# Optimization experiments

Hardware: AMD Instinct MI355X
Metric: run time of the kernel (lower is better)

Reference implementation:

```python
import jax, jax.numpy as jnp
import numpy as np

# dims: batch, time, in-feat, nodes, hidden, out-feat, filter taps, readout widths
BATCH, T, F, N, H, G = 8, 64, 8, 4096, 32, 32
K1, K2 = 3, 3
R1, R2 = 64, 8


def lsigf(h, S, x):
    """K-tap graph filter (LSIGF, E=1): h (Fout,K,Fin), S (N,N), x (B,Fin,N) -> (B,Fout,N)."""
    K = h.shape[1]
    xs = [x]
    for _ in range(K - 1):  # K is small and static
        xs.append(jnp.einsum('nm,bfm->bfn', S, xs[-1]))
    xk = jnp.stack(xs, axis=1)  # B,K,Fin,N
    return jnp.einsum('gkf,bkfn->bgn', h, xk)


def setup_inputs() -> dict:
    key = jax.random.key(0)
    ks = jax.random.split(key, 20)
    def p(k, shape, scale):
        return jax.random.normal(k, shape, dtype=jnp.float32) * scale
    x = jax.random.normal(ks[0], (BATCH, T, F, N), dtype=jnp.float32)
    z0 = jax.random.normal(ks[1], (BATCH, H, N), dtype=jnp.float32)  # random initial hidden state
    S = jax.random.normal(ks[2], (N, N), dtype=jnp.float32) / jnp.sqrt(jnp.float32(N))  # GSO, O(1) spectral norm
    sA = 1.0 / np.sqrt(K1 * F); sB = 1.0 / np.sqrt(K1 * H); sO = 1.0 / np.sqrt(K2 * H)
    return dict(
        x=x, z0=z0, S=S,
        # main hidden-state filters
        A=p(ks[3], (H, K1, F), sA), Bw=p(ks[4], (H, K1, H), sB), bz=p(ks[5], (H, 1), 0.1),
        # input (update) time-gate filters
        Ca=p(ks[6], (H, K1, F), sA), Cb=p(ks[7], (H, K1, H), sB), bc=p(ks[8], (H, 1), 0.1),
        # forget time-gate filters
        Da=p(ks[9], (H, K1, F), sA), Db=p(ks[10], (H, K1, H), sB), bd=p(ks[11], (H, 1), 0.1),
        # output graph filter
        Wout=p(ks[12], (G, K2, H), sO), bout=p(ks[13], (G, 1), 0.1),
        # local per-node readout MLP G -> R1 -> R2
        W1=p(ks[14], (R1, G), 1.0 / np.sqrt(G)), b1=p(ks[15], (R1,), 0.1),
        W2=p(ks[16], (R2, R1), 1.0 / np.sqrt(R1)), b2=p(ks[17], (R2,), 0.1),
    )


def reference(x, z0, S, A, Bw, bz, Ca, Cb, bc, Da, Db, bd, Wout, bout, W1, b1, W2, b2):
    Bsz = x.shape[0]
    xt_seq = jnp.moveaxis(x, 1, 0)  # T,B,F,N

    def step(z, xt):
        # scalar-per-(batch,time) gates: sigmoid of gate graph filters, pooled over nodes+features
        u = jax.nn.sigmoid(lsigf(Ca, S, xt) + lsigf(Cb, S, z) + bc).mean(axis=(1, 2))[:, None, None]
        f = jax.nn.sigmoid(lsigf(Da, S, xt) + lsigf(Db, S, z) + bd).mean(axis=(1, 2))[:, None, None]
        znew = jnp.tanh(u * lsigf(A, S, xt) + f * lsigf(Bw, S, z) + bz)
        return znew, znew

    _, zs = jax.lax.scan(step, z0, xt_seq)  # T,B,H,N
    z = jnp.moveaxis(zs, 0, 1).reshape(Bsz * T, H, N)
    yOut = jnp.tanh(lsigf(Wout, S, z) + bout).reshape(Bsz, T, G, N)  # nonlinearityOutput = tanh
    y = jnp.moveaxis(yOut, 2, 3)  # B,T,N,G  (local per-node readout)
    y = jax.nn.relu(y @ W1.T + b1) @ W2.T + b2  # B,T,N,R2
    return jnp.moveaxis(y, 3, 2)  # B,T,R2,N
```

## Files before the change

### kernel.cpp

```cpp
#include <hip/hip_runtime.h>
#include <hip/hip_bf16.h>
#include <cstdio>

typedef __attribute__((ext_vector_type(4))) float f32x4;
typedef __attribute__((ext_vector_type(8))) short bf16x8;

__device__ __forceinline__ short f2b(float f) {
  unsigned u = __builtin_bit_cast(unsigned, f);
  unsigned r = (u + 0x7FFFu + ((u >> 16) & 1u)) >> 16;
  return (short)r;
}
__device__ __forceinline__ float b2f(short s) {
  union { unsigned u; float f; } c;
  c.u = ((unsigned)(unsigned short)s) << 16;
  return c.f;
}
__device__ __forceinline__ float sigm(float x) { return 1.f / (1.f + __expf(-x)); }
__device__ __forceinline__ float tanh_f(float x) {
  float e = __expf(2.f * x);
  return 1.f - 2.f / (e + 1.f);
}

#define GLOAD16(gp, lp) \
  __builtin_amdgcn_global_load_lds((__attribute__((address_space(1))) const void*)(gp), \
                                   (__attribute__((address_space(3))) void*)(lp), 16, 0, 0)


__global__ void conv_k(const float* __restrict__ in, short* __restrict__ out, int n8) {
  int i = blockIdx.x * 256 + threadIdx.x;
  if (i >= n8) return;
  size_t base = (size_t)i * 8;
  f32x4 a = *(const f32x4*)(in + base), b = *(const f32x4*)(in + base + 4);
  bf16x8 v;
#pragma unroll
  for (int j = 0; j < 4; ++j) { v[j] = f2b(a[j]); v[4 + j] = f2b(b[j]); }
  *(bf16x8*)(out + base) = v;
}

__global__ void transpose_k(const float* __restrict__ in, short* __restrict__ out) {
  __shared__ float tile[32][33];
  int bx = blockIdx.x * 32, by = blockIdx.y * 32;
  int tx = threadIdx.x, ty = threadIdx.y;
  for (int i = ty; i < 32; i += 8)
    tile[i][tx] = in[(size_t)(by + i) * 4096 + bx + tx];
  __syncthreads();
  for (int i = ty; i < 32; i += 8)
    out[(size_t)(bx + i) * 4096 + by + tx] = f2b(tile[tx][i]);
}

template <int AF32>
__global__ __launch_bounds__(256) void gemm_pre(const void* __restrict__ Av,
                                                const short* __restrict__ Bt,
                                                short* __restrict__ C,
                                                int K, int ldc) {
  __shared__ __align__(16) short As[128][72];
  __shared__ __align__(16) short Bs[128][72];
  const int tid = threadIdx.x;
  const int lane = tid & 63, wave = tid >> 6;
  const int wm = wave >> 1, wn = wave & 1;
  const size_t m0 = (size_t)blockIdx.y * 128, n0 = (size_t)blockIdx.x * 128;
  const int r16 = lane & 15, g4 = lane >> 4;

  f32x4 acc[4][4];
#pragma unroll
  for (int mi = 0; mi < 4; ++mi)
#pragma unroll
    for (int ni = 0; ni < 4; ++ni) acc[mi][ni] = (f32x4)0.f;

  for (int kt = 0; kt < K; kt += 64) {
#pragma unroll
    for (int r = 0; r < 4; ++r) {
      int idx = r * 256 + tid;
      int row = idx >> 3;
      int kin = (idx & 7) * 8;
      if (AF32) {
        const float* A = (const float*)Av;
        const float* p = &A[(m0 + row) * (size_t)K + kt + kin];
        f32x4 a = *(const f32x4*)p, b = *(const f32x4*)(p + 4);
        bf16x8 v;
#pragma unroll
        for (int j = 0; j < 4; ++j) { v[j] = f2b(a[j]); v[4 + j] = f2b(b[j]); }
        *(bf16x8*)&As[row][kin] = v;
      } else {
        const short* A = (const short*)Av;
        *(bf16x8*)&As[row][kin] = *(const bf16x8*)&A[(m0 + row) * (size_t)K + kt + kin];
      }
      *(bf16x8*)&Bs[row][kin] = *(const bf16x8*)&Bt[(n0 + row) * (size_t)K + kt + kin];
    }
    __syncthreads();
#pragma unroll
    for (int ks = 0; ks < 2; ++ks) {
      bf16x8 af[4], bfr[4];
#pragma unroll
      for (int i = 0; i < 4; ++i) {
        af[i]  = *(const bf16x8*)&As[wm * 64 + i * 16 + r16][ks * 32 + g4 * 8];
        bfr[i] = *(const bf16x8*)&Bs[wn * 64 + i * 16 + r16][ks * 32 + g4 * 8];
      }
#pragma unroll
      for (int mi = 0; mi < 4; ++mi)
#pragma unroll
        for (int ni = 0; ni < 4; ++ni)
          acc[mi][ni] = __builtin_amdgcn_mfma_f32_16x16x32_bf16(af[mi], bfr[ni], acc[mi][ni], 0, 0, 0);
    }
    __syncthreads();
  }
#pragma unroll
  for (int mi = 0; mi < 4; ++mi) {
#pragma unroll
    for (int ni = 0; ni < 4; ++ni) {
      size_t row0 = m0 + wm * 64 + mi * 16 + g4 * 4;
      size_t col  = n0 + wn * 64 + ni * 16 + r16;
#pragma unroll
      for (int r = 0; r < 4; ++r)
        C[(row0 + r) * (size_t)ldc + col] = f2b(acc[mi][ni][r]);
    }
  }
}

__global__ __launch_bounds__(512, 1) void step_fused(
    const short* __restrict__ zbuf, const short* __restrict__ Scat,
    const float* __restrict__ x, const short* __restrict__ xsh,
    const float* __restrict__ Ca, const float* __restrict__ Cb, const float* __restrict__ bc,
    const float* __restrict__ Da, const float* __restrict__ Db, const float* __restrict__ bd,
    const float* __restrict__ Af, const float* __restrict__ Bw,
    const float* __restrict__ Wout, const float* __restrict__ bout,
    const float* __restrict__ W1, const float* __restrict__ b1,
    const float* __restrict__ W2, const float* __restrict__ b2,
    float* __restrict__ zab, float* __restrict__ gacc,
    float* __restrict__ out, int t) {
  __shared__ __align__(16) char smem[143072];
  short* AbB = (short*)smem;
  short* BbB = (short*)(smem + 49152);
  short* Cs  = (short*)smem;
  short* zs  = (short*)(smem + 18432);
  float* Fu  = (float*)(smem + 73728);
  float* Fd  = (float*)(smem + 89088);
  float* Fb  = (float*)(smem + 104448);
  float* Fa  = (float*)(smem + 116736);
  float* Wc  = (float*)(smem + 119808);
  float* W1L = (float*)(smem + 132096);
  float* W2L = (float*)(smem + 140288);
  float* bcs   = (float*)(smem + 142336);
  float* bds   = (float*)(smem + 142464);
  float* boutL = (float*)(smem + 142592);
  float* b1L   = (float*)(smem + 142720);
  float* b2L   = (float*)(smem + 142976);
  float* red   = (float*)(smem + 143008);

  const int tid = threadIdx.x, lane = tid & 63, w = tid >> 6;
  const int wm = w >> 1, wn = w & 1;
  const int r16 = lane & 15, g4 = lane >> 4;
  const int lrow8 = lane >> 3;
  const int lslot = (lane & 7) ^ lrow8;
  const int swz = r16 & 7;
  const int mhalf = blockIdx.x >> 7, ntile = blockIdx.x & 127;
  const int m0 = mhalf << 7, n0 = ntile << 5;

  for (int i = tid; i < 3840; i += 512) {
    int j = i >> 5, h = i & 31; float fu, fd;
    if (j < 96) { int k = j >> 5, hh = j & 31;
      fu = Cb[(h * 3 + k) * 32 + hh]; fd = Db[(h * 3 + k) * 32 + hh]; }
    else { int jj = j - 96, k = jj >> 3, f = jj & 7;
      fu = Ca[(h * 3 + k) * 8 + f];  fd = Da[(h * 3 + k) * 8 + f]; }
    Fu[i] = fu; Fd[i] = fd;
  }
  for (int i = tid; i < 3072; i += 512) { int j = i >> 5, h = i & 31, k = j >> 5, hh = j & 31;
    Fb[i] = Bw[(h * 3 + k) * 32 + hh]; }
  for (int i = tid; i < 768;  i += 512) { int j = i >> 5, h = i & 31, k = j >> 3, f = j & 7;
    Fa[i] = Af[(h * 3 + k) * 8 + f]; }
  for (int i = tid; i < 3072; i += 512) { int j = i >> 5, g = i & 31, k = j >> 5, hh = j & 31;
    Wc[i] = Wout[(g * 3 + k) * 32 + hh]; }
  for (int i = tid; i < 2048; i += 512) { int r1 = i >> 5, g = i & 31; W1L[i] = W1[r1 * 32 + g]; }
  if (tid < 512) { int r1 = tid >> 3, r = tid & 7; W2L[tid] = W2[r * 64 + r1]; }
  if (tid < 32) { bcs[tid] = bc[tid]; bds[tid] = bd[tid]; boutL[tid] = bout[tid]; }
  if (tid < 64) b1L[tid] = b1[tid];
  if (tid < 8)  b2L[tid] = b2[tid];
  __syncthreads();

  const short* z = zbuf + (size_t)(t & 1) * 1048576;

  f32x4 acc[2][2];
  acc[0][0] = acc[0][1] = acc[1][0] = acc[1][1] = (f32x4)0.f;
  auto stage = [&](int bs, int kt) {
#pragma unroll
    for (int i = 0; i < 2; ++i) {
      int chunk = w * 2 + i, row = chunk * 8 + lrow8;
      GLOAD16(&z[(size_t)(m0 + row) * 4096 + kt + lslot * 8], &AbB[bs * 8192 + chunk * 512]);
    }
    { int row = w * 8 + lrow8;
      int grow = (row < 32) ? (n0 + row) : (4064 + n0 + row);
      GLOAD16(&Scat[(size_t)grow * 4096 + kt + lslot * 8], &BbB[bs * 4096 + w * 512]); }
  };
  stage(0, 0);
  stage(1, 64);
  for (int i = 0; i < 64; ++i) {
    if (i < 63) { asm volatile("s_waitcnt vmcnt(3)" ::: "memory"); }
    else        { asm volatile("s_waitcnt vmcnt(0)" ::: "memory"); }
    __builtin_amdgcn_s_barrier();
    __builtin_amdgcn_sched_barrier(0);
    if (i + 2 < 64) stage((i + 2) % 3, (i + 2) * 64);
    const int cur = i % 3;
#pragma unroll
    for (int ks = 0; ks < 2; ++ks) {
      const int so = ((ks * 4 + g4) ^ swz) * 8;
      bf16x8 af[2], bb[2];
#pragma unroll
      for (int ii = 0; ii < 2; ++ii) {
        af[ii] = *(const bf16x8*)&AbB[cur * 8192 + (wm * 32 + ii * 16 + r16) * 64 + so];
        bb[ii] = *(const bf16x8*)&BbB[cur * 4096 + (wn * 32 + ii * 16 + r16) * 64 + so];
      }
#pragma unroll
      for (int mi = 0; mi < 2; ++mi)
#pragma unroll
        for (int ni = 0; ni < 2; ++ni)
          acc[mi][ni] = __builtin_amdgcn_mfma_f32_16x16x32_bf16(af[mi], bb[ni], acc[mi][ni], 0, 0, 0);
    }
  }
  __syncthreads();

#pragma unroll
  for (int mi = 0; mi < 2; ++mi)
#pragma unroll
    for (int ni = 0; ni < 2; ++ni) {
      int row0 = wm * 32 + mi * 16 + g4 * 4, col = wn * 32 + ni * 16 + r16;
#pragma unroll
      for (int rr = 0; rr < 4; ++rr)
        Cs[(row0 + rr) * 72 + col] = f2b(acc[mi][ni][rr]);
    }
  { int row = tid >> 2, c0 = (tid & 3) * 8;
    *(bf16x8*)&zs[row * 40 + c0] = *(const bf16x8*)&z[(size_t)(m0 + row) * 4096 + n0 + c0]; }
  __syncthreads();

  if (t >= 1 && tid < 128) {
    int b_loc = tid >> 5, nn = tid & 31;
    int b_glob = (mhalf << 2) + b_loc;
    f32x4 oa[8];
#pragma unroll
    for (int q = 0; q < 8; ++q) oa[q] = (f32x4)0.f;
    for (int j = 0; j < 96; ++j) {
      int k = j >> 5, hh = j & 31;
      float v = (k == 0) ? b2f(zs[(b_loc * 32 + hh) * 40 + nn])
                         : b2f(Cs[(b_loc * 32 + hh) * 72 + (k - 1) * 32 + nn]);
#pragma unroll
      for (int q = 0; q < 8; ++q) oa[q] += (*(const f32x4*)&Wc[j * 32 + q * 4]) * v;
    }
    f32x4 y[8];
#pragma unroll
    for (int q = 0; q < 8; ++q)
#pragma unroll
      for (int c = 0; c < 4; ++c) y[q][c] = tanh_f(oa[q][c] + boutL[q * 4 + c]);
    f32x4 o0 = { b2L[0], b2L[1], b2L[2], b2L[3] };
    f32x4 o1 = { b2L[4], b2L[5], b2L[6], b2L[7] };
    for (int r1 = 0; r1 < 64; ++r1) {
      f32x4 p = y[0] * (*(const f32x4*)&W1L[r1 * 32]);
#pragma unroll
      for (int q = 1; q < 8; ++q) p += y[q] * (*(const f32x4*)&W1L[r1 * 32 + q * 4]);
      float hv = b1L[r1] + p[0] + p[1] + p[2] + p[3];
      hv = fmaxf(hv, 0.f);
      o0 += (*(const f32x4*)&W2L[r1 * 8]) * hv;
      o1 += (*(const f32x4*)&W2L[r1 * 8 + 4]) * hv;
    }
    size_t obase = ((size_t)(b_glob * 64 + (t - 1)) * 8) * 4096 + n0 + nn;
#pragma unroll
    for (int rr = 0; rr < 4; ++rr) {
      out[obase + (size_t)rr * 4096]       = o0[rr];
      out[obase + (size_t)(4 + rr) * 4096] = o1[rr];
    }
  }

  if (t < 64) {
    int nn = tid & 31; int q = tid >> 5; int b_loc = q >> 2; int h0 = (q & 3) * 8;
    int b_glob = (mhalf << 2) + b_loc;
    int n = n0 + nn;
    f32x4 zaA = (f32x4)0.f, zaB = (f32x4)0.f, zbA = (f32x4)0.f, zbB = (f32x4)0.f;
    f32x4 guA = *(const f32x4*)&bcs[h0], guB = *(const f32x4*)&bcs[h0 + 4];
    f32x4 gdA = *(const f32x4*)&bds[h0], gdB = *(const f32x4*)&bds[h0 + 4];
    for (int j = 0; j < 96; ++j) {
      int k = j >> 5, hh = j & 31;
      float v = (k == 0) ? b2f(zs[(b_loc * 32 + hh) * 40 + nn])
                         : b2f(Cs[(b_loc * 32 + hh) * 72 + (k - 1) * 32 + nn]);
      guA += (*(const f32x4*)&Fu[j * 32 + h0]) * v;  guB += (*(const f32x4*)&Fu[j * 32 + h0 + 4]) * v;
      gdA += (*(const f32x4*)&Fd[j * 32 + h0]) * v;  gdB += (*(const f32x4*)&Fd[j * 32 + h0 + 4]) * v;
      zbA += (*(const f32x4*)&Fb[j * 32 + h0]) * v;  zbB += (*(const f32x4*)&Fb[j * 32 + h0 + 4]) * v;
    }
    size_t xr = ((size_t)b_glob * 64 + t) * 8;
    for (int j = 0; j < 24; ++j) {
      int k = j >> 3, f = j & 7;
      float v = (k == 0) ? x[(xr + f) * 4096 + n]
                         : b2f(xsh[(xr + f) * 8192 + (size_t)(k - 1) * 4096 + n]);
      guA += (*(const f32x4*)&Fu[(96 + j) * 32 + h0]) * v;  guB += (*(const f32x4*)&Fu[(96 + j) * 32 + h0 + 4]) * v;
      gdA += (*(const f32x4*)&Fd[(96 + j) * 32 + h0]) * v;  gdB += (*(const f32x4*)&Fd[(96 + j) * 32 + h0 + 4]) * v;
      zaA += (*(const f32x4*)&Fa[j * 32 + h0]) * v;         zaB += (*(const f32x4*)&Fa[j * 32 + h0 + 4]) * v;
    }
    float su = 0.f, sd = 0.f;
    size_t zr = (size_t)(b_glob * 32 + h0) * 4096 + n;
#pragma unroll
    for (int i = 0; i < 4; ++i) {
      su += sigm(guA[i]) + sigm(guB[i]);
      sd += sigm(gdA[i]) + sigm(gdB[i]);
      zab[zr + (size_t)i * 4096]                 = zaA[i];
      zab[zr + (size_t)(4 + i) * 4096]           = zaB[i];
      zab[1048576 + zr + (size_t)i * 4096]       = zbA[i];
      zab[1048576 + zr + (size_t)(4 + i) * 4096] = zbB[i];
    }
#pragma unroll
    for (int off = 32; off; off >>= 1) { su += __shfl_down(su, off); sd += __shfl_down(sd, off); }
    if (lane == 0) { red[w * 2] = su; red[w * 2 + 1] = sd; }
    __syncthreads();
    if (tid < 4) {
      int par = t & 1, bg = (mhalf << 2) + tid;
      atomicAdd(&gacc[par * 16 + bg],     red[4 * tid] + red[4 * tid + 2]);
      atomicAdd(&gacc[par * 16 + 8 + bg], red[4 * tid + 1] + red[4 * tid + 3]);
    }
  }
}

__global__ __launch_bounds__(256) void update_kernel(
    const float* __restrict__ zab, float* __restrict__ gacc,
    const float* __restrict__ bz, short* __restrict__ zout, int t) {
  const int par = t & 1;
  if (blockIdx.x == 0 && threadIdx.x < 16) gacc[(par ^ 1) * 16 + threadIdx.x] = 0.f;
  size_t idx = (size_t)blockIdx.x * 256 + threadIdx.x;
  size_t base = idx * 8;
  int row = (int)(base >> 12);
  int b = row >> 5, h = row & 31;
  float u  = gacc[par * 16 + b]     * (1.f / 131072.f);
  float fg = gacc[par * 16 + 8 + b] * (1.f / 131072.f);
  float bzv = bz[h];
  f32x4 za0 = *(const f32x4*)(zab + base),           za1 = *(const f32x4*)(zab + base + 4);
  f32x4 zb0 = *(const f32x4*)(zab + 1048576 + base), zb1 = *(const f32x4*)(zab + 1048576 + base + 4);
  bf16x8 ov;
#pragma unroll
  for (int i = 0; i < 4; ++i) {
    ov[i]     = f2b(tanh_f(u * za0[i] + fg * zb0[i] + bzv));
    ov[4 + i] = f2b(tanh_f(u * za1[i] + fg * zb1[i] + bzv));
  }
  *(bf16x8*)(zout + base) = ov;
}

extern "C" void kernel_launch(void* const* d_in, const int* in_sizes, int n_in,
                              void* d_out, int out_size, void* d_ws, size_t ws_size,
                              hipStream_t stream) {
  const float* x    = (const float*)d_in[0];
  const float* z0   = (const float*)d_in[1];
  const float* S    = (const float*)d_in[2];
  const float* Af   = (const float*)d_in[3];
  const float* Bw   = (const float*)d_in[4];
  const float* bz   = (const float*)d_in[5];
  const float* Ca   = (const float*)d_in[6];
  const float* Cb   = (const float*)d_in[7];
  const float* bc   = (const float*)d_in[8];
  const float* Da   = (const float*)d_in[9];
  const float* Db   = (const float*)d_in[10];
  const float* bd   = (const float*)d_in[11];
  const float* Wout = (const float*)d_in[12];
  const float* bo   = (const float*)d_in[13];
  const float* W1   = (const float*)d_in[14];
  const float* b1   = (const float*)d_in[15];
  const float* W2   = (const float*)d_in[16];
  const float* b2   = (const float*)d_in[17];
  float* out = (float*)d_out;

  char* w = (char*)d_ws;
  short* Scat = (short*)w; w += (size_t)8192 * 4096 * 2;
  short* xsh  = (short*)w; w += (size_t)4096 * 8192 * 2;
  short* zbuf = (short*)w; w += (size_t)2 * 1048576 * 2;
  float* zab  = (float*)w; w += (size_t)2 * 1048576 * 4;
  float* gacc = (float*)w; w += 256;
  size_t need = (size_t)(w - (char*)d_ws);
  if (ws_size < need) {
    fprintf(stderr, "kernel_launch: WS TOO SMALL need=%zu have=%zu -- NOT LAUNCHING\n",
            need, ws_size);
    return;
  }

  short* STt = xsh;

  conv_k<<<512, 256, 0, stream>>>(z0, zbuf, 131072);
  conv_k<<<8192, 256, 0, stream>>>(S, Scat, 2097152);
  transpose_k<<<dim3(128, 128), dim3(32, 8), 0, stream>>>(S, STt);
  gemm_pre<0><<<dim3(32, 32), 256, 0, stream>>>(Scat, STt, Scat + (size_t)4096 * 4096, 4096, 4096);
  gemm_pre<1><<<dim3(64, 32), 256, 0, stream>>>(x, Scat, xsh, 4096, 8192);
  hipMemsetAsync(gacc, 0, 256, stream);

  for (int t = 0; t <= 64; ++t) {
    short* znxt = zbuf + (size_t)((t + 1) & 1) * 1048576;
    step_fused<<<256, 512, 0, stream>>>(zbuf, Scat, x, xsh,
                                        Ca, Cb, bc, Da, Db, bd, Af, Bw,
                                        Wout, bo, W1, b1, W2, b2,
                                        zab, gacc, out, t);
    if (t < 64)
      update_kernel<<<512, 256, 0, stream>>>(zab, gacc, bz, znxt, t);
  }
}
```

Baseline: 6.178 ms.

## Use direct-to-LDS swizzled loads in precompute GEMM and bf16 filter weights in step kernel

The precompute GEMMs now fill LDS with global_load_lds 16-byte transfers into an XOR-swizzled layout, replacing register-staged copies into padded arrays. The A operand, when fp32, is converted per row-pair. In the fused step kernel the filter, output, and readout weights move to bf16 in LDS with an h-group-major layout, shrinking shared memory and halving LDS read traffic in the per-node loops. Rounding the weights to bf16 costs accuracy, and the unpacking adds ALU work. A leftover no-op loop is also present.

```diff
diff --git a/kernel.cpp b/kernel.cpp
--- a/kernel.cpp
+++ b/kernel.cpp
@@ -14,6 +14,12 @@
   union { unsigned u; float f; } c;
   c.u = ((unsigned)(unsigned short)s) << 16;
   return c.f;
+}
+__device__ __forceinline__ f32x4 blo(bf16x8 v) {
+  f32x4 r; r[0] = b2f(v[0]); r[1] = b2f(v[1]); r[2] = b2f(v[2]); r[3] = b2f(v[3]); return r;
+}
+__device__ __forceinline__ f32x4 bhi(bf16x8 v) {
+  f32x4 r; r[0] = b2f(v[4]); r[1] = b2f(v[5]); r[2] = b2f(v[6]); r[3] = b2f(v[7]); return r;
 }
 __device__ __forceinline__ float sigm(float x) { return 1.f / (1.f + __expf(-x)); }
 __device__ __forceinline__ float tanh_f(float x) {
@@ -49,17 +55,20 @@
 }
 
 template <int AF32>
-__global__ __launch_bounds__(256) void gemm_pre(const void* __restrict__ Av,
-                                                const short* __restrict__ Bt,
-                                                short* __restrict__ C,
-                                                int K, int ldc) {
-  __shared__ __align__(16) short As[128][72];
-  __shared__ __align__(16) short Bs[128][72];
-  const int tid = threadIdx.x;
-  const int lane = tid & 63, wave = tid >> 6;
-  const int wm = wave >> 1, wn = wave & 1;
+__global__ __launch_bounds__(256) void gemm_pre2(const void* __restrict__ Av,
+                                                 const short* __restrict__ Bt,
+                                                 short* __restrict__ C,
+                                                 int K, int ldc) {
+  __shared__ __align__(16) short As[128 * 64];
+  __shared__ __align__(16) short Bs[128 * 64];
+  const int tid = threadIdx.x, lane = tid & 63, w = tid >> 6;
+  const int wm = w >> 1, wn = w & 1;
+  const int r16 = lane & 15, g4 = lane >> 4;
   const size_t m0 = (size_t)blockIdx.y * 128, n0 = (size_t)blockIdx.x * 128;
-  const int r16 = lane & 15, g4 = lane >> 4;
+  const int lrow8 = lane >> 3;
+  const int lslot = (lane & 7) ^ lrow8;
+  const int swz = r16 & 7;
+  const int arow = tid >> 1, acol0 = (tid & 1) * 32, aslotb = (tid & 1) * 4;
 
   f32x4 acc[4][4];
 #pragma unroll
@@ -67,40 +76,49 @@
 #pragma unroll
     for (int ni = 0; ni < 4; ++ni) acc[mi][ni] = (f32x4)0.f;
 
+  const float* A32 = (const float*)Av;
   for (int kt = 0; kt < K; kt += 64) {
 #pragma unroll
-    for (int r = 0; r < 4; ++r) {
-      int idx = r * 256 + tid;
-      int row = idx >> 3;
-      int kin = (idx & 7) * 8;
-      if (AF32) {
-        const float* A = (const float*)Av;
-        const float* p = &A[(m0 + row) * (size_t)K + kt + kin];
-        f32x4 a = *(const f32x4*)p, b = *(const f32x4*)(p + 4);
+    for (int i = 0; i < 4; ++i) {
+      int chunk = w * 4 + i, row = chunk * 8 + lrow8;
+      GLOAD16(&Bt[(size_t)(n0 + row) * K + kt + lslot * 8], &Bs[chunk * 512]);
+    }
+    if (AF32) {
+      f32x4 st[8];
+#pragma unroll
+      for (int j = 0; j < 8; ++j)
+        st[j] = *(const f32x4*)&A32[(m0 + arow) * (size_t)K + kt + acol0 + j * 4];
+#pragma unroll
+      for (int s = 0; s < 4; ++s) {
         bf16x8 v;
 #pragma unroll
-        for (int j = 0; j < 4; ++j) { v[j] = f2b(a[j]); v[4 + j] = f2b(b[j]); }
-        *(bf16x8*)&As[row][kin] = v;
-      } else {
-        const short* A = (const short*)Av;
-        *(bf16x8*)&As[row][kin] = *(const bf16x8*)&A[(m0 + row) * (size_t)K + kt + kin];
+        for (int e = 0; e < 4; ++e) { v[e] = f2b(st[s * 2][e]); v[4 + e] = f2b(st[s * 2 + 1][e]); }
+        int ps = (aslotb + s) ^ (arow & 7);
+        *(bf16x8*)&As[arow * 64 + ps * 8] = v;
       }
-      *(bf16x8*)&Bs[row][kin] = *(const bf16x8*)&Bt[(n0 + row) * (size_t)K + kt + kin];
+    } else {
+      const short* A = (const short*)Av;
+#pragma unroll
+      for (int i = 0; i < 4; ++i) {
+        int chunk = w * 4 + i, row = chunk * 8 + lrow8;
+        GLOAD16(&A[(size_t)(m0 + row) * K + kt + lslot * 8], &As[chunk * 512]);
+      }
     }
     __syncthreads();
 #pragma unroll
     for (int ks = 0; ks < 2; ++ks) {
-      bf16x8 af[4], bfr[4];
+      const int so = ((ks * 4 + g4) ^ swz) * 8;
+      bf16x8 af[4], bf[4];
 #pragma unroll
       for (int i = 0; i < 4; ++i) {
-        af[i]  = *(const bf16x8*)&As[wm * 64 + i * 16 + r16][ks * 32 + g4 * 8];
-        bfr[i] = *(const bf16x8*)&Bs[wn * 64 + i * 16 + r16][ks * 32 + g4 * 8];
+        af[i] = *(const bf16x8*)&As[(wm * 64 + i * 16 + r16) * 64 + so];
+        bf[i] = *(const bf16x8*)&Bs[(wn * 64 + i * 16 + r16) * 64 + so];
       }
 #pragma unroll
       for (int mi = 0; mi < 4; ++mi)
 #pragma unroll
         for (int ni = 0; ni < 4; ++ni)
-          acc[mi][ni] = __builtin_amdgcn_mfma_f32_16x16x32_bf16(af[mi], bfr[ni], acc[mi][ni], 0, 0, 0);
+          acc[mi][ni] = __builtin_amdgcn_mfma_f32_16x16x32_bf16(af[mi], bf[ni], acc[mi][ni], 0, 0, 0);
     }
     __syncthreads();
   }
@@ -128,24 +146,23 @@
     const float* __restrict__ W2, const float* __restrict__ b2,
     float* __restrict__ zab, float* __restrict__ gacc,
     float* __restrict__ out, int t) {
-  __shared__ __align__(16) char smem[143072];
+  __shared__ __align__(16) char smem[108768];
   short* AbB = (short*)smem;
   short* BbB = (short*)(smem + 49152);
   short* Cs  = (short*)smem;
   short* zs  = (short*)(smem + 18432);
-  float* Fu  = (float*)(smem + 73728);
-  float* Fd  = (float*)(smem + 89088);
-  float* Fb  = (float*)(smem + 104448);
-  float* Fa  = (float*)(smem + 116736);
-  float* Wc  = (float*)(smem + 119808);
-  float* W1L = (float*)(smem + 132096);
-  float* W2L = (float*)(smem + 140288);
-  float* bcs   = (float*)(smem + 142336);
-  float* bds   = (float*)(smem + 142464);
-  float* boutL = (float*)(smem + 142592);
-  float* b1L   = (float*)(smem + 142720);
-  float* b2L   = (float*)(smem + 142976);
-  float* red   = (float*)(smem + 143008);
+  short* FuH = (short*)(smem + 73728);
+  short* FdH = (short*)(smem + 81408);
+  short* FzH = (short*)(smem + 89088);
+  short* WcH = (short*)(smem + 96768);
+  short* W1H = (short*)(smem + 102912);
+  short* W2H = (short*)(smem + 107008);
+  float* bcs   = (float*)(smem + 108032);
+  float* bds   = (float*)(smem + 108160);
+  float* boutL = (float*)(smem + 108288);
+  float* b1L   = (float*)(smem + 108416);
+  float* b2L   = (float*)(smem + 108672);
+  float* red   = (float*)(smem + 108704);
 
   const int tid = threadIdx.x, lane = tid & 63, w = tid >> 6;
   const int wm = w >> 1, wn = w & 1;
@@ -157,21 +174,20 @@
   const int m0 = mhalf << 7, n0 = ntile << 5;
 
   for (int i = tid; i < 3840; i += 512) {
-    int j = i >> 5, h = i & 31; float fu, fd;
+    int hg = i / 960, rem = i % 960, j = rem >> 3, e = rem & 7;
+    int h = hg * 8 + e;
+    float fu, fd, fz;
     if (j < 96) { int k = j >> 5, hh = j & 31;
-      fu = Cb[(h * 3 + k) * 32 + hh]; fd = Db[(h * 3 + k) * 32 + hh]; }
+      fu = Cb[(h * 3 + k) * 32 + hh]; fd = Db[(h * 3 + k) * 32 + hh]; fz = Bw[(h * 3 + k) * 32 + hh]; }
     else { int jj = j - 96, k = jj >> 3, f = jj & 7;
-      fu = Ca[(h * 3 + k) * 8 + f];  fd = Da[(h * 3 + k) * 8 + f]; }
-    Fu[i] = fu; Fd[i] = fd;
-  }
-  for (int i = tid; i < 3072; i += 512) { int j = i >> 5, h = i & 31, k = j >> 5, hh = j & 31;
-    Fb[i] = Bw[(h * 3 + k) * 32 + hh]; }
-  for (int i = tid; i < 768;  i += 512) { int j = i >> 5, h = i & 31, k = j >> 3, f = j & 7;
-    Fa[i] = Af[(h * 3 + k) * 8 + f]; }
+      fu = Ca[(h * 3 + k) * 8 + f];  fd = Da[(h * 3 + k) * 8 + f];  fz = Af[(h * 3 + k) * 8 + f]; }
+    FuH[i] = f2b(fu); FdH[i] = f2b(fd); FzH[i] = f2b(fz);
+  }
   for (int i = tid; i < 3072; i += 512) { int j = i >> 5, g = i & 31, k = j >> 5, hh = j & 31;
-    Wc[i] = Wout[(g * 3 + k) * 32 + hh]; }
-  for (int i = tid; i < 2048; i += 512) { int r1 = i >> 5, g = i & 31; W1L[i] = W1[r1 * 32 + g]; }
-  if (tid < 512) { int r1 = tid >> 3, r = tid & 7; W2L[tid] = W2[r * 64 + r1]; }
+    WcH[i] = f2b(Wout[(g * 3 + k) * 32 + hh]); }
+  for (int i = tid; i < 2048; i += 512) WcH == nullptr ? void() : void();
+  for (int i = tid; i < 2048; i += 512) W1H[i] = f2b(W1[i]);
+  if (tid < 512) { int r1 = tid >> 3, r = tid & 7; W2H[tid] = f2b(W2[r * 64 + r1]); }
   if (tid < 32) { bcs[tid] = bc[tid]; bds[tid] = bd[tid]; boutL[tid] = bout[tid]; }
   if (tid < 64) b1L[tid] = b1[tid];
   if (tid < 8)  b2L[tid] = b2[tid];
@@ -241,8 +257,14 @@
       int k = j >> 5, hh = j & 31;
       float v = (k == 0) ? b2f(zs[(b_loc * 32 + hh) * 40 + nn])
                          : b2f(Cs[(b_loc * 32 + hh) * 72 + (k - 1) * 32 + nn]);
-#pragma unroll
-      for (int q = 0; q < 8; ++q) oa[q] += (*(const f32x4*)&Wc[j * 32 + q * 4]) * v;
+      bf16x8 w0 = *(const bf16x8*)&WcH[j * 32];
+      bf16x8 w1 = *(const bf16x8*)&WcH[j * 32 + 8];
+      bf16x8 w2 = *(const bf16x8*)&WcH[j * 32 + 16];
+      bf16x8 w3 = *(const bf16x8*)&WcH[j * 32 + 24];
+      oa[0] += blo(w0) * v; oa[1] += bhi(w0) * v;
+      oa[2] += blo(w1) * v; oa[3] += bhi(w1) * v;
+      oa[4] += blo(w2) * v; oa[5] += bhi(w2) * v;
+      oa[6] += blo(w3) * v; oa[7] += bhi(w3) * v;
     }
     f32x4 y[8];
 #pragma unroll
@@ -252,13 +274,16 @@
     f32x4 o0 = { b2L[0], b2L[1], b2L[2], b2L[3] };
     f32x4 o1 = { b2L[4], b2L[5], b2L[6], b2L[7] };
     for (int r1 = 0; r1 < 64; ++r1) {
-      f32x4 p = y[0] * (*(const f32x4*)&W1L[r1 * 32]);
-#pragma unroll
-      for (int q = 1; q < 8; ++q) p += y[q] * (*(const f32x4*)&W1L[r1 * 32 + q * 4]);
-      float hv = b1L[r1] + p[0] + p[1] + p[2] + p[3];
-      hv = fmaxf(hv, 0.f);
-      o0 += (*(const f32x4*)&W2L[r1 * 8]) * hv;
-      o1 += (*(const f32x4*)&W2L[r1 * 8 + 4]) * hv;
+      bf16x8 a0 = *(const bf16x8*)&W1H[r1 * 32];
+      bf16x8 a1 = *(const bf16x8*)&W1H[r1 * 32 + 8];
+      bf16x8 a2 = *(const bf16x8*)&W1H[r1 * 32 + 16];
+      bf16x8 a3 = *(const bf16x8*)&W1H[r1 * 32 + 24];
+      f32x4 p = y[0] * blo(a0) + y[1] * bhi(a0) + y[2] * blo(a1) + y[3] * bhi(a1)
+              + y[4] * blo(a2) + y[5] * bhi(a2) + y[6] * blo(a3) + y[7] * bhi(a3);
+      float hv = fmaxf(b1L[r1] + p[0] + p[1] + p[2] + p[3], 0.f);
+      bf16x8 wv = *(const bf16x8*)&W2H[r1 * 8];
+      o0 += blo(wv) * hv;
+      o1 += bhi(wv) * hv;
     }
     size_t obase = ((size_t)(b_glob * 64 + (t - 1)) * 8) * 4096 + n0 + nn;
 #pragma unroll
@@ -269,9 +294,12 @@
   }
 
   if (t < 64) {
-    int nn = tid & 31; int q = tid >> 5; int b_loc = q >> 2; int h0 = (q & 3) * 8;
+    int nn = tid & 31; int q = tid >> 5; int b_loc = q >> 2; int hg = q & 3; int h0 = hg * 8;
     int b_glob = (mhalf << 2) + b_loc;
     int n = n0 + nn;
+    const short* FuB = &FuH[hg * 960];
+    const short* FdB = &FdH[hg * 960];
+    const short* FzB = &FzH[hg * 960];
     f32x4 zaA = (f32x4)0.f, zaB = (f32x4)0.f, zbA = (f32x4)0.f, zbB = (f32x4)0.f;
     f32x4 guA = *(const f32x4*)&bcs[h0], guB = *(const f32x4*)&bcs[h0 + 4];
     f32x4 gdA = *(const f32x4*)&bds[h0], gdB = *(const f32x4*)&bds[h0 + 4];
@@ -279,18 +307,24 @@
       int k = j >> 5, hh = j & 31;
       float v = (k == 0) ? b2f(zs[(b_loc * 32 + hh) * 40 + nn])
                          : b2f(Cs[(b_loc * 32 + hh) * 72 + (k - 1) * 32 + nn]);
-      guA += (*(const f32x4*)&Fu[j * 32 + h0]) * v;  guB += (*(const f32x4*)&Fu[j * 32 + h0 + 4]) * v;
-      gdA += (*(const f32x4*)&Fd[j * 32 + h0]) * v;  gdB += (*(const f32x4*)&Fd[j * 32 + h0 + 4]) * v;
-      zbA += (*(const f32x4*)&Fb[j * 32 + h0]) * v;  zbB += (*(const f32x4*)&Fb[j * 32 + h0 + 4]) * v;
+      bf16x8 fu = *(const bf16x8*)&FuB[j * 8];
+      bf16x8 fd = *(const bf16x8*)&FdB[j * 8];
+      bf16x8 fz = *(const bf16x8*)&FzB[j * 8];
+      guA += blo(fu) * v; guB += bhi(fu) * v;
+      gdA += blo(fd) * v; gdB += bhi(fd) * v;
+      zbA += blo(fz) * v; zbB += bhi(fz) * v;
     }
     size_t xr = ((size_t)b_glob * 64 + t) * 8;
-    for (int j = 0; j < 24; ++j) {
-      int k = j >> 3, f = j & 7;
+    for (int j = 96; j < 120; ++j) {
+      int jj = j - 96, k = jj >> 3, f = jj & 7;
       float v = (k == 0) ? x[(xr + f) * 4096 + n]
                          : b2f(xsh[(xr + f) * 8192 + (size_t)(k - 1) * 4096 + n]);
-      guA += (*(const f32x4*)&Fu[(96 + j) * 32 + h0]) * v;  guB += (*(const f32x4*)&Fu[(96 + j) * 32 + h0 + 4]) * v;
-      gdA += (*(const f32x4*)&Fd[(96 + j) * 32 + h0]) * v;  gdB += (*(const f32x4*)&Fd[(96 + j) * 32 + h0 + 4]) * v;
-      zaA += (*(const f32x4*)&Fa[j * 32 + h0]) * v;         zaB += (*(const f32x4*)&Fa[j * 32 + h0 + 4]) * v;
+      bf16x8 fu = *(const bf16x8*)&FuB[j * 8];
+      bf16x8 fd = *(const bf16x8*)&FdB[j * 8];
+      bf16x8 fz = *(const bf16x8*)&FzB[j * 8];
+      guA += blo(fu) * v; guB += bhi(fu) * v;
+      gdA += blo(fd) * v; gdB += bhi(fd) * v;
+      zaA += blo(fz) * v; zaB += bhi(fz) * v;
     }
     float su = 0.f, sd = 0.f;
     size_t zr = (size_t)(b_glob * 32 + h0) * 4096 + n;
@@ -379,8 +413,8 @@
   conv_k<<<512, 256, 0, stream>>>(z0, zbuf, 131072);
   conv_k<<<8192, 256, 0, stream>>>(S, Scat, 2097152);
   transpose_k<<<dim3(128, 128), dim3(32, 8), 0, stream>>>(S, STt);
-  gemm_pre<0><<<dim3(32, 32), 256, 0, stream>>>(Scat, STt, Scat + (size_t)4096 * 4096, 4096, 4096);
-  gemm_pre<1><<<dim3(64, 32), 256, 0, stream>>>(x, Scat, xsh, 4096, 8192);
+  gemm_pre2<0><<<dim3(32, 32), 256, 0, stream>>>(Scat, STt, Scat + (size_t)4096 * 4096, 4096, 4096);
+  gemm_pre2<1><<<dim3(64, 32), 256, 0, stream>>>(x, Scat, xsh, 4096, 8192);
   hipMemsetAsync(gacc, 0, 256, stream);
 
   for (int t = 0; t <= 64; ++t) {
```

Measured after the change: 6.419 ms. 1.04x slower.
